# Optimization experiments

Measured on AMD Instinct MI355X. Metric: run time of the kernel, lower is better.

The kernel has to match this reference:

```python
import jax, jax.numpy as jnp
import numpy as np

N_NODES = 160_000
N_EDGES = 640_000
N_GRAPHS = 8_000
IN_FEATS = 74
HID = 63
MAX_DEG = 10
PRED_HID = 128
PRED_DIM = 256
BN_EPS = 1e-5
N_LAYERS = 3
PARAM_NAMES = ['W0', 'b0', 'gamma0', 'beta0', 'W1', 'b1', 'gamma1', 'beta1', 'W2', 'b2', 'gamma2', 'beta2', 'W_ng', 'b_ng', 'W_tr', 'b_tr']


def setup_inputs() -> dict:
    key = jax.random.key(0)
    ks = jax.random.split(key, 20)
    inp = {}
    inp['feats'] = jax.random.normal(ks[0], (N_NODES, IN_FEATS), dtype=jnp.float32)
    inp['src'] = jax.random.randint(ks[1], (N_EDGES,), 0, N_NODES, dtype=jnp.int32)
    inp['dst'] = jax.random.randint(ks[2], (N_EDGES,), 0, N_NODES, dtype=jnp.int32)
    # sorted graph membership: 20 nodes per graph (batched molecular graphs)
    inp['graph_ids'] = jnp.repeat(jnp.arange(N_GRAPHS, dtype=jnp.int32), N_NODES // N_GRAPHS)
    dims = [IN_FEATS, HID, HID, HID]
    for l in range(N_LAYERS):
        fi, fo = dims[l], dims[l + 1]
        inp[f'W{l}'] = jax.random.normal(ks[3 + l], (MAX_DEG, fi, fo), dtype=jnp.float32) / np.float32(np.sqrt(fi))
        inp[f'b{l}'] = jnp.zeros((MAX_DEG, fo), dtype=jnp.float32)
        inp[f'gamma{l}'] = jnp.ones((fo,), dtype=jnp.float32)
        inp[f'beta{l}'] = jnp.zeros((fo,), dtype=jnp.float32)
    inp['W_ng'] = jax.random.normal(ks[10], (HID, PRED_HID), dtype=jnp.float32) / np.float32(np.sqrt(HID))
    inp['b_ng'] = jnp.zeros((PRED_HID,), dtype=jnp.float32)
    inp['W_tr'] = jax.random.normal(ks[11], (2 * PRED_HID, PRED_DIM), dtype=jnp.float32) / np.float32(np.sqrt(2 * PRED_HID))
    inp['b_tr'] = jnp.zeros((PRED_DIM,), dtype=jnp.float32)
    return inp


def _nf_layer(h, src, dst, deg_idx, W, b, gamma, beta):
    # message passing: sum of neighbor features via copy_u / fn.sum
    neigh = jax.ops.segment_sum(h[src], dst, num_segments=N_NODES)
    tot = h + neigh  # self + neighbor sum (Duvenaud neural fingerprint)
    # degree-bucketed linear: compute all MAX_DEG transforms, select per node by degree
    z_all = jnp.einsum('ni,kio->nko', tot, W) + b  # [N, MAX_DEG, out]
    z = jnp.take_along_axis(z_all, deg_idx[:, None, None], axis=1)[:, 0, :]  # [N, out]
    z = jax.nn.relu(z)
    # batchnorm over nodes (training-mode batch statistics, eps=1e-5)
    mu = jnp.mean(z, axis=0)
    var = jnp.var(z, axis=0)
    return (z - mu) * jax.lax.rsqrt(var + BN_EPS) * gamma + beta


def _forward(feats, src, dst, graph_ids, params):
    # in-degree per node, clamped to [1, MAX_DEG] -> weight bucket index
    deg = jax.ops.segment_sum(jnp.ones((N_EDGES,), jnp.float32), dst, num_segments=N_NODES)
    deg_idx = jnp.clip(deg.astype(jnp.int32), 1, MAX_DEG) - 1
    h = feats
    for l in range(N_LAYERS):
        h = _nf_layer(h, src, dst, deg_idx, params[f'W{l}'], params[f'b{l}'],
                      params[f'gamma{l}'], params[f'beta{l}'])
    # node_to_graph linear
    h = h @ params['W_ng'] + params['b_ng']  # [N, PRED_HID]
    # SumAndMax readout over each graph
    g_sum = jax.ops.segment_sum(h, graph_ids, num_segments=N_GRAPHS)
    g_max = jax.ops.segment_max(h, graph_ids, num_segments=N_GRAPHS)
    g = jnp.tanh(jnp.concatenate([g_sum, g_max], axis=-1))  # [G, 2*PRED_HID]
    return g @ params['W_tr'] + params['b_tr']  # [G, PRED_DIM]


def reference(feats, src, dst, graph_ids, W0, b0, gamma0, beta0, W1, b1, gamma1, beta1, W2, b2, gamma2, beta2, W_ng, b_ng, W_tr, b_tr):
    params = dict(zip(PARAM_NAMES, (W0, b0, gamma0, beta0, W1, b1, gamma1, beta1, W2, b2, gamma2, beta2, W_ng, b_ng, W_tr, b_tr)))
    return _forward(feats, src, dst, graph_ids, params)
```

## Files before the change

kernel.cpp:

```cpp
#include <hip/hip_runtime.h>
#include <stdint.h>
#include <math.h>

static constexpr int NN = 160000;
static constexpr int NE = 640000;
static constexpr int NG = 8000;
static constexpr int FH  = 63;
static constexpr int ZST = 64;
static constexpr int FST = 80;
static constexpr int NB  = 128;
static constexpr int LGRID = 1536;

static constexpr size_t OFF_DEGCNT = 0;
static constexpr size_t OFF_CURSOR = 640000;
static constexpr size_t OFF_BCNT   = 1280000;
static constexpr size_t OFF_SPART  = 1280064;
static constexpr size_t ZERO_BYTES = 1673280;
static constexpr size_t OFF_ROWPTR = 1673280;
static constexpr size_t OFF_BLKSUM = 2313472;
static constexpr size_t OFF_COL    = 2315520;
static constexpr size_t OFF_BLIST  = 4875520;
static constexpr size_t OFF_AFC    = 17675520;
static constexpr size_t OFF_BNG2   = 17709312;
static constexpr size_t OFF_PBLK   = 17709824;
static constexpr size_t OFF_FB     = 17710080;
static constexpr size_t OFF_Z0     = 43310080;
static constexpr size_t OFF_Z1     = 63790080;
static constexpr size_t OFF_WNGF   = OFF_Z1;
static constexpr size_t OFF_WTRF   = OFF_Z1 + 32768;

__device__ __forceinline__ float blo(unsigned u) {
    union { unsigned i; float f; } v; v.i = u << 16; return v.f;
}
__device__ __forceinline__ float bhi(unsigned u) {
    union { unsigned i; float f; } v; v.i = u & 0xffff0000u; return v.f;
}
__device__ __forceinline__ unsigned short f2b(float f) {
    union { float f; unsigned i; } v; v.f = f;
    unsigned r = v.i + 0x7fffu + ((v.i >> 16) & 1u);
    return (unsigned short)(r >> 16);
}
__device__ __forceinline__ void acc8(float* a, uint4 q) {
    a[0] += blo(q.x); a[1] += bhi(q.x);
    a[2] += blo(q.y); a[3] += bhi(q.y);
    a[4] += blo(q.z); a[5] += bhi(q.z);
    a[6] += blo(q.w); a[7] += bhi(q.w);
}

typedef __attribute__((ext_vector_type(8))) short bf16x8;
typedef __attribute__((ext_vector_type(4))) float f32x4;
union U8 { uint4 u; bf16x8 b; };

__global__ void k_cast(const float* __restrict__ feats, unsigned short* __restrict__ fb,
                       const int* __restrict__ dst, int* __restrict__ degcnt) {
    int i = blockIdx.x * 256 + threadIdx.x;
    if (i < NE) atomicAdd(&degcnt[dst[i]], 1);
    if (i >= NN * FST) return;
    int n = i / FST, c = i - n * FST;
    float v = (c < 74) ? feats[n * 74 + c] : 0.f;
    union { float f; unsigned u; } x; x.f = v;
    unsigned r = x.u + 0x7fffu + ((x.u >> 16) & 1u);
    fb[i] = (unsigned short)(r >> 16);
}

__global__ void k_scan1(const int* __restrict__ degcnt, int* __restrict__ row_ptr,
                        int* __restrict__ blksum) {
    __shared__ int s[1024];
    int t = threadIdx.x;
    int i = blockIdx.x * 1024 + t;
    int v = (i < NN) ? degcnt[i] : 0;
    s[t] = v; __syncthreads();
    for (int off = 1; off < 1024; off <<= 1) {
        int x = (t >= off) ? s[t - off] : 0;
        __syncthreads();
        s[t] += x;
        __syncthreads();
    }
    if (i < NN) row_ptr[i + 1] = s[t];
    if (t == 1023) blksum[blockIdx.x] = s[t];
}

__global__ void k_scan2(int* __restrict__ blksum, int nblk) {
    __shared__ int s[256];
    int t = threadIdx.x;
    int v = (t < nblk) ? blksum[t] : 0;
    s[t] = v; __syncthreads();
    for (int off = 1; off < 256; off <<= 1) {
        int x = (t >= off) ? s[t - off] : 0;
        __syncthreads();
        s[t] += x;
        __syncthreads();
    }
    if (t < nblk) blksum[t] = s[t] - v;
}

__global__ void k_scan3(int* __restrict__ row_ptr, const int* __restrict__ blksum) {
    int t = threadIdx.x;
    int i = blockIdx.x * 1024 + t;
    if (i < NN) row_ptr[i + 1] += blksum[blockIdx.x];
    if (i == 0) row_ptr[0] = 0;
}

__global__ void __launch_bounds__(1024) k_bucket(
        const int* __restrict__ degcnt, const int* __restrict__ row_ptr,
        int* __restrict__ bcnt, int2* __restrict__ blist,
        int* __restrict__ pblk, int* __restrict__ ctr) {
    __shared__ int scnt[10], sbase[10];
    __shared__ int sLast;
    int tid = threadIdx.x;
    if (tid < 10) scnt[tid] = 0;
    __syncthreads();
    int n = blockIdx.x * 1024 + tid;
    int k = 0, pos = 0;
    bool v = (n < NN);
    int rp = 0;
    if (v) {
        int d = degcnt[n];
        rp = row_ptr[n];
        k = (d < 1) ? 0 : ((d > 10) ? 9 : d - 1);
        pos = atomicAdd(&scnt[k], 1);
    }
    __syncthreads();
    if (tid < 10) sbase[tid] = scnt[tid] ? atomicAdd(&bcnt[tid], scnt[tid]) : 0;
    __syncthreads();
    if (v) blist[k * NN + sbase[k] + pos] = make_int2(n, rp);

    if (tid == 0) {
        __threadfence();
        sLast = (atomicAdd(ctr, 1) == (int)gridDim.x - 1) ? 1 : 0;
    }
    __syncthreads();
    if (sLast && tid == 0) {
        __threadfence();
        const volatile int* bc = bcnt;
        int s = 0; pblk[0] = 0;
        for (int kk = 0; kk < 10; ++kk) { s += (bc[kk] + NB - 1) / NB; pblk[kk + 1] = s; }
    }
}

__global__ void k_fill(const int* __restrict__ src, const int* __restrict__ dst,
                       const int* __restrict__ row_ptr, int* __restrict__ cursor,
                       int* __restrict__ col) {
    int e = blockIdx.x * 256 + threadIdx.x;
    if (e >= NE) return;
    int d = dst[e];
    int pos = row_ptr[d] + atomicAdd(&cursor[d], 1);
    col[pos] = src[e];
}

template<int FI, int IST, bool AFF>
__global__ void __launch_bounds__(512, 4) k_layer(
    const unsigned short* __restrict__ in,
    const float* __restrict__ aff,
    const int* __restrict__ row_ptr, const int* __restrict__ col,
    const int* __restrict__ bcnt, const int2* __restrict__ blist,
    const int* __restrict__ pblk,
    const float* __restrict__ W, const float* __restrict__ B,
    unsigned short* __restrict__ zout, float* __restrict__ spart)
{
    constexpr int CH = IST / 8;
    __shared__ float sW[FI * 63 + 64];
    __shared__ float sTot[8][IST][8];
    __shared__ int   sN[8][8];
    __shared__ float sRed[2][8][64];

    int b = blockIdx.x;
    if (b >= pblk[10]) return;
    int k = 0;
#pragma unroll
    for (int i = 1; i <= 9; ++i) k += (b >= pblk[i]) ? 1 : 0;
    int base = (b - pblk[k]) * NB;
    int cnt = bcnt[k];
    if (base >= cnt) return;

    int tid = threadIdx.x;
    int wave = tid >> 6, lane = tid & 63;
    int t = lane >> 3, r = lane & 7;

    const float* Wk = W + (size_t)k * FI * 63;
#pragma unroll 4
    for (int i = tid; i < FI * 63; i += 512) sW[i] = Wk[i];
    __syncthreads();

    const uint4* inq = (const uint4*)in;
    float bterm = (lane < 63) ? B[k * 63 + lane] : 0.f;
    float lsum = 0.f, lsq = 0.f;

#pragma unroll 1
    for (int it = 0; it < NB / 64; ++it) {
        int idx = base + it * 64 + wave * 8 + t;
        if (base + it * 64 >= cnt) break;
        bool val = (idx < cnt);
        int2 bl = blist[k * NN + (val ? idx : (cnt - 1))];
        int n = bl.x, rs = bl.y;
        int dg = (k >= 1 && k <= 8) ? (k + 1) : (row_ptr[n + 1] - rs);
        if (r == 0) sN[wave][t] = val ? n : -1;

        float a[8] = {0.f, 0.f, 0.f, 0.f, 0.f, 0.f, 0.f, 0.f};
        {
            uint4 q = inq[(size_t)n * CH + r];
            acc8(a, q);
        }
        int d = 0;
#pragma unroll 1
        for (; d + 4 <= dg; d += 4) {
            int c0 = col[rs + d], c1 = col[rs + d + 1];
            int c2 = col[rs + d + 2], c3 = col[rs + d + 3];
            uint4 q0 = inq[(size_t)c0 * CH + r];
            uint4 q1 = inq[(size_t)c1 * CH + r];
            uint4 q2 = inq[(size_t)c2 * CH + r];
            uint4 q3 = inq[(size_t)c3 * CH + r];
            acc8(a, q0); acc8(a, q1); acc8(a, q2); acc8(a, q3);
        }
#pragma unroll 1
        for (; d < dg; ++d) {
            int c = col[rs + d];
            uint4 q = inq[(size_t)c * CH + r];
            acc8(a, q);
        }

        if constexpr (IST == 80) {
            float e2[8] = {0.f, 0.f, 0.f, 0.f, 0.f, 0.f, 0.f, 0.f};
            if (r < 2) {
                uint4 q = inq[(size_t)n * CH + 8 + r];
                acc8(e2, q);
                int d2 = 0;
#pragma unroll 1
                for (; d2 < dg; ++d2) {
                    int c = col[rs + d2];
                    uint4 p = inq[(size_t)c * CH + 8 + r];
                    acc8(e2, p);
                }
#pragma unroll
                for (int j = 0; j < 8; ++j) sTot[wave][64 + 8 * r + j][t] = e2[j];
            }
        }

        if constexpr (AFF) {
            const float4* af = (const float4*)aff;
            float4 A0 = af[2 * r], A1 = af[2 * r + 1];
            float4 C0 = af[16 + 2 * r], C1 = af[16 + 2 * r + 1];
            float dp1 = (float)(dg + 1);
            a[0] = A0.x * a[0] + dp1 * C0.x;  a[1] = A0.y * a[1] + dp1 * C0.y;
            a[2] = A0.z * a[2] + dp1 * C0.z;  a[3] = A0.w * a[3] + dp1 * C0.w;
            a[4] = A1.x * a[4] + dp1 * C1.x;  a[5] = A1.y * a[5] + dp1 * C1.y;
            a[6] = A1.z * a[6] + dp1 * C1.z;  a[7] = A1.w * a[7] + dp1 * C1.w;
        }

#pragma unroll
        for (int j = 0; j < 8; ++j) sTot[wave][8 * r + j][t] = a[j];

        float acc[8];
#pragma unroll
        for (int i = 0; i < 8; ++i) acc[i] = bterm;
#pragma unroll 4
        for (int j = 0; j < FI; ++j) {
            float w = sW[j * 63 + lane];
            float4 u = *(const float4*)&sTot[wave][j][0];
            float4 v = *(const float4*)&sTot[wave][j][4];
            acc[0] = fmaf(u.x, w, acc[0]); acc[1] = fmaf(u.y, w, acc[1]);
            acc[2] = fmaf(u.z, w, acc[2]); acc[3] = fmaf(u.w, w, acc[3]);
            acc[4] = fmaf(v.x, w, acc[4]); acc[5] = fmaf(v.y, w, acc[5]);
            acc[6] = fmaf(v.z, w, acc[6]); acc[7] = fmaf(v.w, w, acc[7]);
        }

#pragma unroll
        for (int tt = 0; tt < 8; ++tt) {
            int nn = sN[wave][tt];
            float z = fmaxf(acc[tt], 0.f);
            if (nn >= 0 && lane < 63) {
                zout[(size_t)nn * ZST + lane] = f2b(z);
                lsum += z; lsq += z * z;
            }
        }
    }

    sRed[0][wave][lane] = lsum;
    sRed[1][wave][lane] = lsq;
    __syncthreads();
    if (wave == 0 && lane < 63) {
        float s = 0.f, q = 0.f;
#pragma unroll
        for (int w8 = 0; w8 < 8; ++w8) {
            s += sRed[0][w8][lane];
            q += sRed[1][w8][lane];
        }
        float* sp = spart + (size_t)(blockIdx.x & 255) * 128;
        atomicAdd(&sp[lane], s);
        atomicAdd(&sp[64 + lane], q);
    }
}

__global__ void k_bn(const float* __restrict__ spart, const float* __restrict__ gamma,
                     const float* __restrict__ beta, float* __restrict__ afc) {
    __shared__ double sd[512];
    int o = blockIdx.x;
    int t = threadIdx.x;
    sd[t]       = (double)spart[t * 128 + o];
    sd[256 + t] = (double)spart[t * 128 + 64 + o];
    __syncthreads();
#pragma unroll
    for (int off = 128; off > 0; off >>= 1) {
        if (t < off) { sd[t] += sd[t + off]; sd[256 + t] += sd[256 + t + off]; }
        __syncthreads();
    }
    if (t == 0) {
        double mu  = sd[0] / NN;
        double var = sd[256] / NN - mu * mu;
        float a = (float)((double)gamma[o] / sqrt(var + 1e-5));
        float c = (float)((double)beta[o] - mu * (double)a);
        afc[o] = a;
        afc[64 + o] = c;
    }
}

__global__ void k_prepw(const float* __restrict__ W_ng, const float* __restrict__ b_ng,
                        const float* __restrict__ afc2, const float* __restrict__ W_tr,
                        unsigned short* __restrict__ WngF, unsigned short* __restrict__ WtrF,
                        float* __restrict__ bng2) {
    int bid = blockIdx.x, tid = threadIdx.x;
    if (bid == 0) {
        if (tid < 128) {
            float acc = b_ng[tid];
            for (int j = 0; j < 63; ++j)
                acc = fmaf(afc2[64 + j], W_ng[j * 128 + tid], acc);
            bng2[tid] = acc;
        }
    } else if (bid <= 64) {
        int idx = (bid - 1) * 256 + tid;
        int j = idx & 7, lane = (idx >> 3) & 63;
        int nt = (idx >> 9) & 7, kb = idx >> 12;
        int k = (kb & 1) * 32 + ((lane >> 4) << 3) + j;
        int col = nt * 16 + (lane & 15);
        float w = (k < 63) ? afc2[k] * W_ng[k * 128 + col] : 0.f;
        unsigned short hi = f2b(w);
        if (kb < 2) WngF[idx] = hi;
        else        WngF[idx] = f2b(w - blo(hi));
    } else {
        int idx = (bid - 65) * 256 + tid;
        int j = idx & 7, lane = (idx >> 3) & 63;
        int kb = (idx >> 9) & 7, nt = idx >> 12;
        int k = kb * 32 + ((lane >> 4) << 3) + j;
        int col = nt * 16 + (lane & 15);
        WtrF[idx] = f2b(W_tr[k * 256 + col]);
    }
}

__global__ void __launch_bounds__(256, 2) k_graph(
    const unsigned short* __restrict__ Z2, const unsigned short* __restrict__ WngF,
    const float* __restrict__ bng2, const unsigned short* __restrict__ WtrF,
    const float* __restrict__ b_tr, float* __restrict__ out)
{
    __shared__ unsigned short sW[16384];
    __shared__ float sT[16 * 256];
    __shared__ float sB[128];

    int tid = threadIdx.x;
    int wave = tid >> 6, lane = tid & 63;
    int gl15 = lane & 15, grp = lane >> 4;

    {
        const uint4* srcq = (const uint4*)WngF;
        uint4* dstq = (uint4*)sW;
#pragma unroll
        for (int i = 0; i < 8; ++i) dstq[tid + 256 * i] = srcq[tid + 256 * i];
    }
    if (tid < 128) sB[tid] = bng2[tid];
    __syncthreads();

    int nodeBase = blockIdx.x * 320 + wave * 80;
    const uint4* zq = (const uint4*)Z2;
    uint4 a0[5], a1[5];
#pragma unroll
    for (int m = 0; m < 5; ++m) {
        size_t row = (size_t)(nodeBase + m * 16 + gl15) * 8;
        a0[m] = zq[row + grp];
        a1[m] = zq[row + 4 + grp];
    }
    if (grp == 3) {
#pragma unroll
        for (int m = 0; m < 5; ++m) a1[m].w &= 0xffffu;
    }

    const uint4* swq = (const uint4*)sW;
    const float NEGI = -3.0e38f;

#pragma unroll 1
    for (int nt = 0; nt < 8; ++nt) {
        U8 b0, b1, b2, b3;
        b0.u = swq[(0 * 8 + nt) * 64 + lane];
        b1.u = swq[(1 * 8 + nt) * 64 + lane];
        b2.u = swq[(2 * 8 + nt) * 64 + lane];
        b3.u = swq[(3 * 8 + nt) * 64 + lane];

        f32x4 ac[5];
#pragma unroll
        for (int m = 0; m < 5; ++m) {
            U8 xa0, xa1; xa0.u = a0[m]; xa1.u = a1[m];
            f32x4 c = {0.f, 0.f, 0.f, 0.f};
            c = __builtin_amdgcn_mfma_f32_16x16x32_bf16(xa0.b, b0.b, c, 0, 0, 0);
            c = __builtin_amdgcn_mfma_f32_16x16x32_bf16(xa1.b, b1.b, c, 0, 0, 0);
            c = __builtin_amdgcn_mfma_f32_16x16x32_bf16(xa0.b, b2.b, c, 0, 0, 0);
            c = __builtin_amdgcn_mfma_f32_16x16x32_bf16(xa1.b, b3.b, c, 0, 0, 0);
            ac[m] = c;
        }

        float s[4] = {0.f, 0.f, 0.f, 0.f};
        float x[4] = {NEGI, NEGI, NEGI, NEGI};
        bool cA = lane < 16, cB = lane < 32, cC = lane < 48;
#pragma unroll
        for (int r = 0; r < 4; ++r) {
            float v0 = ac[0][r]; s[0] += v0; x[0] = fmaxf(x[0], v0);
            float v4 = ac[4][r]; s[3] += v4; x[3] = fmaxf(x[3], v4);
            float v1 = ac[1][r]; float v1a = cA ? v1 : 0.f;
            s[0] += v1a; s[1] += v1 - v1a;
            x[0] = fmaxf(x[0], cA ? v1 : NEGI); x[1] = fmaxf(x[1], cA ? NEGI : v1);
            float v2 = ac[2][r]; float v2a = cB ? v2 : 0.f;
            s[1] += v2a; s[2] += v2 - v2a;
            x[1] = fmaxf(x[1], cB ? v2 : NEGI); x[2] = fmaxf(x[2], cB ? NEGI : v2);
            float v3 = ac[3][r]; float v3a = cC ? v3 : 0.f;
            s[2] += v3a; s[3] += v3 - v3a;
            x[2] = fmaxf(x[2], cC ? v3 : NEGI); x[3] = fmaxf(x[3], cC ? NEGI : v3);
        }
#pragma unroll
        for (int g = 0; g < 4; ++g) {
            s[g] += __shfl_xor(s[g], 16);
            s[g] += __shfl_xor(s[g], 32);
            x[g] = fmaxf(x[g], __shfl_xor(x[g], 16));
            x[g] = fmaxf(x[g], __shfl_xor(x[g], 32));
        }
        if (lane < 16) {
            int c = nt * 16 + lane;
            float bb = sB[c];
#pragma unroll
            for (int g = 0; g < 4; ++g) {
                int row = wave * 4 + g;
                int swz = (row & 7) << 2;
                sT[(row * 256 + c) ^ swz]       = tanhf(s[g] + 20.f * bb);
                sT[(row * 256 + 128 + c) ^ swz] = tanhf(x[g] + bb);
            }
        }
    }
    __syncthreads();

    U8 pa[8];
    {
        int swz = (gl15 & 7) << 2;
#pragma unroll
        for (int kb = 0; kb < 8; ++kb) {
            int k8 = kb * 32 + grp * 8;
            float4 t0 = *(const float4*)&sT[(gl15 * 256 + k8) ^ swz];
            float4 t1 = *(const float4*)&sT[(gl15 * 256 + k8 + 4) ^ swz];
            unsigned u0 = (unsigned)f2b(t0.x) | ((unsigned)f2b(t0.y) << 16);
            unsigned u1 = (unsigned)f2b(t0.z) | ((unsigned)f2b(t0.w) << 16);
            unsigned u2 = (unsigned)f2b(t1.x) | ((unsigned)f2b(t1.y) << 16);
            unsigned u3 = (unsigned)f2b(t1.z) | ((unsigned)f2b(t1.w) << 16);
            pa[kb].u = make_uint4(u0, u1, u2, u3);
        }
    }
    const uint4* wtq = (const uint4*)WtrF;
    size_t gbase = (size_t)blockIdx.x * 16 * 256;
#pragma unroll 2
    for (int i = 0; i < 4; ++i) {
        int nt = wave * 4 + i;
        f32x4 c = {0.f, 0.f, 0.f, 0.f};
#pragma unroll
        for (int kb = 0; kb < 8; ++kb) {
            U8 b; b.u = wtq[(nt * 8 + kb) * 64 + lane];
            c = __builtin_amdgcn_mfma_f32_16x16x32_bf16(pa[kb].b, b.b, c, 0, 0, 0);
        }
        int d = nt * 16 + gl15;
        float btv = b_tr[d];
#pragma unroll
        for (int r = 0; r < 4; ++r) {
            int row = grp * 4 + r;
            out[gbase + (size_t)row * 256 + d] = c[r] + btv;
        }
    }
}

extern "C" void kernel_launch(void* const* d_in, const int* in_sizes, int n_in,
                              void* d_out, int out_size, void* d_ws, size_t ws_size,
                              hipStream_t stream) {
    const float* feats = (const float*)d_in[0];
    const int*   src   = (const int*)d_in[1];
    const int*   dst   = (const int*)d_in[2];
    const float* W0 = (const float*)d_in[4];
    const float* b0 = (const float*)d_in[5];
    const float* g0 = (const float*)d_in[6];
    const float* be0 = (const float*)d_in[7];
    const float* W1 = (const float*)d_in[8];
    const float* b1 = (const float*)d_in[9];
    const float* g1 = (const float*)d_in[10];
    const float* be1 = (const float*)d_in[11];
    const float* W2 = (const float*)d_in[12];
    const float* b2 = (const float*)d_in[13];
    const float* g2 = (const float*)d_in[14];
    const float* be2 = (const float*)d_in[15];
    const float* Wng = (const float*)d_in[16];
    const float* bng = (const float*)d_in[17];
    const float* Wtr = (const float*)d_in[18];
    const float* btr = (const float*)d_in[19];
    float* out = (float*)d_out;

    char* ws = (char*)d_ws;
    int*    degcnt  = (int*)(ws + OFF_DEGCNT);
    int*    cursor  = (int*)(ws + OFF_CURSOR);
    int*    bcnt    = (int*)(ws + OFF_BCNT);
    int*    ctr     = bcnt + 10;
    float*  spart   = (float*)(ws + OFF_SPART);
    int*    row_ptr = (int*)(ws + OFF_ROWPTR);
    int*    blksum  = (int*)(ws + OFF_BLKSUM);
    int*    col     = (int*)(ws + OFF_COL);
    int2*   blist   = (int2*)(ws + OFF_BLIST);
    float*  afc     = (float*)(ws + OFF_AFC);
    float*  bng2    = (float*)(ws + OFF_BNG2);
    int*    pblk    = (int*)(ws + OFF_PBLK);
    unsigned short* Fb = (unsigned short*)(ws + OFF_FB);
    unsigned short* Z0 = (unsigned short*)(ws + OFF_Z0);
    unsigned short* Z1 = (unsigned short*)(ws + OFF_Z1);
    unsigned short* Z2 = Z0;
    unsigned short* WngF = (unsigned short*)(ws + OFF_WNGF);
    unsigned short* WtrF = (unsigned short*)(ws + OFF_WTRF);

    hipMemsetAsync(d_ws, 0, ZERO_BYTES, stream);

    k_cast<<<NN * FST / 256, 256, 0, stream>>>(feats, Fb, dst, degcnt);
    k_scan1<<<157, 1024, 0, stream>>>(degcnt, row_ptr, blksum);
    k_scan2<<<1, 256, 0, stream>>>(blksum, 157);
    k_scan3<<<157, 1024, 0, stream>>>(row_ptr, blksum);
    k_bucket<<<157, 1024, 0, stream>>>(degcnt, row_ptr, bcnt, blist, pblk, ctr);
    k_fill<<<NE / 256, 256, 0, stream>>>(src, dst, row_ptr, cursor, col);

    k_layer<74, FST, false><<<LGRID, 512, 0, stream>>>(
        Fb, nullptr, row_ptr, col, bcnt, blist, pblk, W0, b0, Z0, spart);
    k_bn<<<63, 256, 0, stream>>>(spart, g0, be0, afc);
    k_layer<63, ZST, true><<<LGRID, 512, 0, stream>>>(
        Z0, afc, row_ptr, col, bcnt, blist, pblk, W1, b1, Z1, spart + 256 * 128);
    k_bn<<<63, 256, 0, stream>>>(spart + 256 * 128, g1, be1, afc + 128);
    k_layer<63, ZST, true><<<LGRID, 512, 0, stream>>>(
        Z1, afc + 128, row_ptr, col, bcnt, blist, pblk, W2, b2, Z2, spart + 2 * 256 * 128);
    k_bn<<<63, 256, 0, stream>>>(spart + 2 * 256 * 128, g2, be2, afc + 256);

    k_prepw<<<321, 256, 0, stream>>>(Wng, bng, afc + 256, Wtr, WngF, WtrF, bng2);
    k_graph<<<NG / 16, 256, 0, stream>>>(Z2, WngF, bng2, WtrF, btr, out);
}
```

Baseline: 419.0 us.

## Fuse CSR build: decoupled scan with last-block finish, merge bucket and fill kernels

Folds the block-sum scan into k_scan1 using a last-block-done counter, and merges the scan fixup, degree bucketing and CSR column fill into one kernel (k_buckfill). Each row offset is computed on the fly from the partial scan plus the block prefix. This cuts the preprocessing from five launches to two, removing launch gaps and one full row_ptr pass. In exchange it relies on atomic-counter completion detection, needs an extra partial row_ptr buffer in the shifted workspace layout, and the fill work now runs in 1024-thread blocks.

Result: no change. 415.5 us (-0.8%).

```diff
diff --git a/kernel.cpp b/kernel.cpp
--- a/kernel.cpp
+++ b/kernel.cpp
@@ -17,15 +17,16 @@
 static constexpr size_t OFF_SPART  = 1280064;
 static constexpr size_t ZERO_BYTES = 1673280;
 static constexpr size_t OFF_ROWPTR = 1673280;
-static constexpr size_t OFF_BLKSUM = 2313472;
-static constexpr size_t OFF_COL    = 2315520;
-static constexpr size_t OFF_BLIST  = 4875520;
-static constexpr size_t OFF_AFC    = 17675520;
-static constexpr size_t OFF_BNG2   = 17709312;
-static constexpr size_t OFF_PBLK   = 17709824;
-static constexpr size_t OFF_FB     = 17710080;
-static constexpr size_t OFF_Z0     = 43310080;
-static constexpr size_t OFF_Z1     = 63790080;
+static constexpr size_t OFF_ROWPTRP= 2313472;
+static constexpr size_t OFF_BLKSUM = 2953728;
+static constexpr size_t OFF_COL    = 2955776;
+static constexpr size_t OFF_BLIST  = 5515776;
+static constexpr size_t OFF_AFC    = 18315776;
+static constexpr size_t OFF_BNG2   = 18316544;
+static constexpr size_t OFF_PBLK   = 18317056;
+static constexpr size_t OFF_FB     = 18317184;
+static constexpr size_t OFF_Z0     = 43917184;
+static constexpr size_t OFF_Z1     = 64397184;
 static constexpr size_t OFF_WNGF   = OFF_Z1;
 static constexpr size_t OFF_WTRF   = OFF_Z1 + 32768;
 
@@ -63,9 +64,11 @@
     fb[i] = (unsigned short)(r >> 16);
 }
 
-__global__ void k_scan1(const int* __restrict__ degcnt, int* __restrict__ row_ptr,
-                        int* __restrict__ blksum) {
+__global__ void __launch_bounds__(1024) k_scan1(
+        const int* __restrict__ degcnt, int* __restrict__ row_ptrP,
+        int* __restrict__ blksum, int* __restrict__ ctr) {
     __shared__ int s[1024];
+    __shared__ int sLast;
     int t = threadIdx.x;
     int i = blockIdx.x * 1024 + t;
     int v = (i < NN) ? degcnt[i] : 0;
@@ -76,76 +79,81 @@
         s[t] += x;
         __syncthreads();
     }
-    if (i < NN) row_ptr[i + 1] = s[t];
+    if (i < NN) row_ptrP[i + 1] = s[t];
     if (t == 1023) blksum[blockIdx.x] = s[t];
-}
-
-__global__ void k_scan2(int* __restrict__ blksum, int nblk) {
-    __shared__ int s[256];
-    int t = threadIdx.x;
-    int v = (t < nblk) ? blksum[t] : 0;
-    s[t] = v; __syncthreads();
-    for (int off = 1; off < 256; off <<= 1) {
-        int x = (t >= off) ? s[t - off] : 0;
-        __syncthreads();
-        s[t] += x;
-        __syncthreads();
-    }
-    if (t < nblk) blksum[t] = s[t] - v;
-}
-
-__global__ void k_scan3(int* __restrict__ row_ptr, const int* __restrict__ blksum) {
-    int t = threadIdx.x;
-    int i = blockIdx.x * 1024 + t;
-    if (i < NN) row_ptr[i + 1] += blksum[blockIdx.x];
-    if (i == 0) row_ptr[0] = 0;
-}
-
-__global__ void __launch_bounds__(1024) k_bucket(
-        const int* __restrict__ degcnt, const int* __restrict__ row_ptr,
-        int* __restrict__ bcnt, int2* __restrict__ blist,
-        int* __restrict__ pblk, int* __restrict__ ctr) {
-    __shared__ int scnt[10], sbase[10];
-    __shared__ int sLast;
-    int tid = threadIdx.x;
-    if (tid < 10) scnt[tid] = 0;
-    __syncthreads();
-    int n = blockIdx.x * 1024 + tid;
-    int k = 0, pos = 0;
-    bool v = (n < NN);
-    int rp = 0;
-    if (v) {
-        int d = degcnt[n];
-        rp = row_ptr[n];
-        k = (d < 1) ? 0 : ((d > 10) ? 9 : d - 1);
-        pos = atomicAdd(&scnt[k], 1);
-    }
-    __syncthreads();
-    if (tid < 10) sbase[tid] = scnt[tid] ? atomicAdd(&bcnt[tid], scnt[tid]) : 0;
-    __syncthreads();
-    if (v) blist[k * NN + sbase[k] + pos] = make_int2(n, rp);
-
-    if (tid == 0) {
+
+    if (t == 0) {
         __threadfence();
         sLast = (atomicAdd(ctr, 1) == (int)gridDim.x - 1) ? 1 : 0;
     }
     __syncthreads();
-    if (sLast && tid == 0) {
+    if (sLast) {
         __threadfence();
-        const volatile int* bc = bcnt;
-        int s = 0; pblk[0] = 0;
-        for (int kk = 0; kk < 10; ++kk) { s += (bc[kk] + NB - 1) / NB; pblk[kk + 1] = s; }
-    }
-}
-
-__global__ void k_fill(const int* __restrict__ src, const int* __restrict__ dst,
-                       const int* __restrict__ row_ptr, int* __restrict__ cursor,
-                       int* __restrict__ col) {
-    int e = blockIdx.x * 256 + threadIdx.x;
-    if (e >= NE) return;
-    int d = dst[e];
-    int pos = row_ptr[d] + atomicAdd(&cursor[d], 1);
-    col[pos] = src[e];
+        int vv = 0;
+        if (t < 256) {
+            const volatile int* bs = blksum;
+            vv = (t < 157) ? bs[t] : 0;
+            s[t] = vv;
+        }
+        __syncthreads();
+        for (int off = 1; off < 256; off <<= 1) {
+            int x = (t >= off && t < 256) ? s[t - off] : 0;
+            __syncthreads();
+            if (t < 256) s[t] += x;
+            __syncthreads();
+        }
+        if (t < 157) blksum[t] = s[t] - vv;
+    }
+}
+
+__global__ void __launch_bounds__(1024) k_buckfill(
+        const int* __restrict__ degcnt, const int* __restrict__ row_ptrP,
+        const int* __restrict__ blksum, int* __restrict__ row_ptr,
+        int* __restrict__ bcnt, int2* __restrict__ blist,
+        const int* __restrict__ src, const int* __restrict__ dst,
+        int* __restrict__ cursor, int* __restrict__ col,
+        int* __restrict__ pblk, int* __restrict__ ctr) {
+    int bid = blockIdx.x, tid = threadIdx.x;
+    if (bid < 157) {
+        __shared__ int scnt[10], sbase[10];
+        __shared__ int sLast;
+        if (tid < 10) scnt[tid] = 0;
+        __syncthreads();
+        int n = bid * 1024 + tid;
+        bool v = (n < NN);
+        int k = 0, pos = 0, rp = 0;
+        if (v) {
+            int d = degcnt[n];
+            k = (d < 1) ? 0 : ((d > 10) ? 9 : d - 1);
+            pos = atomicAdd(&scnt[k], 1);
+            rp = (n == 0) ? 0 : (row_ptrP[n] + blksum[(n - 1) >> 10]);
+            row_ptr[n + 1] = row_ptrP[n + 1] + blksum[n >> 10];
+            if (n == 0) row_ptr[0] = 0;
+        }
+        __syncthreads();
+        if (tid < 10) sbase[tid] = scnt[tid] ? atomicAdd(&bcnt[tid], scnt[tid]) : 0;
+        __syncthreads();
+        if (v) blist[k * NN + sbase[k] + pos] = make_int2(n, rp);
+
+        if (tid == 0) {
+            __threadfence();
+            sLast = (atomicAdd(ctr, 1) == 156) ? 1 : 0;
+        }
+        __syncthreads();
+        if (sLast && tid == 0) {
+            __threadfence();
+            const volatile int* bc = bcnt;
+            int s = 0; pblk[0] = 0;
+            for (int kk = 0; kk < 10; ++kk) { s += (bc[kk] + NB - 1) / NB; pblk[kk + 1] = s; }
+        }
+    } else {
+        int e = (bid - 157) * 1024 + tid;
+        if (e >= NE) return;
+        int d = dst[e];
+        int rpd = (d == 0) ? 0 : (row_ptrP[d] + blksum[(d - 1) >> 10]);
+        int pos = rpd + atomicAdd(&cursor[d], 1);
+        col[pos] = src[e];
+    }
 }
 
 template<int FI, int IST, bool AFF>
@@ -510,6 +518,7 @@
     int*    ctr     = bcnt + 10;
     float*  spart   = (float*)(ws + OFF_SPART);
     int*    row_ptr = (int*)(ws + OFF_ROWPTR);
+    int*    row_ptrP= (int*)(ws + OFF_ROWPTRP);
     int*    blksum  = (int*)(ws + OFF_BLKSUM);
     int*    col     = (int*)(ws + OFF_COL);
     int2*   blist   = (int2*)(ws + OFF_BLIST);
@@ -526,11 +535,10 @@
     hipMemsetAsync(d_ws, 0, ZERO_BYTES, stream);
 
     k_cast<<<NN * FST / 256, 256, 0, stream>>>(feats, Fb, dst, degcnt);
-    k_scan1<<<157, 1024, 0, stream>>>(degcnt, row_ptr, blksum);
-    k_scan2<<<1, 256, 0, stream>>>(blksum, 157);
-    k_scan3<<<157, 1024, 0, stream>>>(row_ptr, blksum);
-    k_bucket<<<157, 1024, 0, stream>>>(degcnt, row_ptr, bcnt, blist, pblk, ctr);
-    k_fill<<<NE / 256, 256, 0, stream>>>(src, dst, row_ptr, cursor, col);
+    k_scan1<<<157, 1024, 0, stream>>>(degcnt, row_ptrP, blksum, ctr + 0);
+    k_buckfill<<<782, 1024, 0, stream>>>(degcnt, row_ptrP, blksum, row_ptr,
+                                         bcnt, blist, src, dst, cursor, col,
+                                         pblk, ctr + 1);
 
     k_layer<74, FST, false><<<LGRID, 512, 0, stream>>>(
         Fb, nullptr, row_ptr, col, bcnt, blist, pblk, W0, b0, Z0, spart);
```
